# Kernel tuning notes

Hardware: AMD Instinct MI355X
Metric: run time of the kernel (lower is better)

The kernel has to match this reference:

```python
import jax, jax.numpy as jnp
import numpy as np


def setup_inputs() -> dict:
    key = jax.random.key(0)
    k1, k2 = jax.random.split(key)
    outputs = jax.random.normal(k1, (256, 8192, 3), dtype=jnp.float32)
    targets = jax.random.normal(k2, (256, 8192, 3), dtype=jnp.float32)
    return {"outputs": outputs, "targets": targets}


def reference(outputs, targets):
    # Flatten to rows of 3-vectors, per the original reshape((-1, 3)).
    o = outputs.reshape(-1, 3)
    t = targets.reshape(-1, 3)
    # Row-wise dot and norms, angle via acos, then mean.
    dot = jnp.sum(o * t, axis=-1)
    cos = dot / (jnp.linalg.norm(o, axis=-1) * jnp.linalg.norm(t, axis=-1))
    angles = jnp.arccos(cos)
    return jnp.mean(angles)
```

## Files before the change

kernel.cpp:

```cpp
#include <hip/hip_runtime.h>
#include <math.h>

#define N_ROWS   (256 * 8192)
#define BLOCK    256
#define ROWS_PER_THREAD 4
#define GRID     (N_ROWS / (BLOCK * ROWS_PER_THREAD))
#define F4_PER_BLOCK (BLOCK * 3)

__device__ __forceinline__ int swz(int j) { return j ^ ((j >> 3) & 7); }

__device__ __forceinline__ float acos_fast(float x) {
    float ax = fabsf(x);
    float s  = sqrtf(fmaxf(0.0f, 1.0f - ax));
    float p  = fmaf(ax, -0.0187293f, 0.0742610f);
    p = fmaf(ax, p, -0.2121144f);
    p = fmaf(ax, p, 1.5707288f);
    float r = s * p;
    return (x >= 0.0f) ? r : (3.14159265358979f - r);
}

__global__ __launch_bounds__(BLOCK) void angle_partial(
    const float* __restrict__ o,
    const float* __restrict__ t,
    float* __restrict__ partial)
{
    __shared__ float4 so[F4_PER_BLOCK];
    __shared__ float4 st[F4_PER_BLOCK];

    const int tx  = threadIdx.x;
    const int bid = blockIdx.x;
    const long base4 = (long)bid * F4_PER_BLOCK;
    const float4* o4 = reinterpret_cast<const float4*>(o);
    const float4* t4 = reinterpret_cast<const float4*>(t);

#pragma unroll
    for (int k = 0; k < 3; ++k) {
        int j = k * BLOCK + tx;
        so[swz(j)] = o4[base4 + j];
        st[swz(j)] = t4[base4 + j];
    }
    __syncthreads();

    float4 a0 = so[swz(3 * tx + 0)];
    float4 a1 = so[swz(3 * tx + 1)];
    float4 a2 = so[swz(3 * tx + 2)];
    float4 b0 = st[swz(3 * tx + 0)];
    float4 b1 = st[swz(3 * tx + 1)];
    float4 b2 = st[swz(3 * tx + 2)];

    float ox[4] = {a0.x, a0.w, a1.z, a2.y};
    float oy[4] = {a0.y, a1.x, a1.w, a2.z};
    float oz[4] = {a0.z, a1.y, a2.x, a2.w};
    float tx_[4] = {b0.x, b0.w, b1.z, b2.y};
    float ty_[4] = {b0.y, b1.x, b1.w, b2.z};
    float tz_[4] = {b0.z, b1.y, b2.x, b2.w};

    float s = 0.0f;
#pragma unroll
    for (int r = 0; r < 4; ++r) {
        float dot = ox[r] * tx_[r] + oy[r] * ty_[r] + oz[r] * tz_[r];
        float no2 = ox[r] * ox[r] + oy[r] * oy[r] + oz[r] * oz[r];
        float nt2 = tx_[r] * tx_[r] + ty_[r] * ty_[r] + tz_[r] * tz_[r];
        float c = dot * rsqrtf(no2) * rsqrtf(nt2);
        c = fminf(1.0f, fmaxf(-1.0f, c));
        s += acos_fast(c);
    }

#pragma unroll
    for (int off = 32; off > 0; off >>= 1)
        s += __shfl_down(s, off, 64);

    __shared__ float waves[BLOCK / 64];
    const int lane = tx & 63;
    const int wid  = tx >> 6;
    if (lane == 0) waves[wid] = s;
    __syncthreads();

    if (tx == 0) {
        float bs = 0.0f;
#pragma unroll
        for (int w = 0; w < BLOCK / 64; ++w) bs += waves[w];
        partial[bid] = bs;
    }
}

__global__ __launch_bounds__(BLOCK) void angle_final(
    const float* __restrict__ partial,
    float* __restrict__ out)
{
    float s = 0.0f;
    for (int i = threadIdx.x; i < GRID; i += BLOCK)
        s += partial[i];

#pragma unroll
    for (int off = 32; off > 0; off >>= 1)
        s += __shfl_down(s, off, 64);

    __shared__ float waves[BLOCK / 64];
    const int lane = threadIdx.x & 63;
    const int wid  = threadIdx.x >> 6;
    if (lane == 0) waves[wid] = s;
    __syncthreads();

    if (threadIdx.x == 0) {
        float total = 0.0f;
#pragma unroll
        for (int w = 0; w < BLOCK / 64; ++w) total += waves[w];
        out[0] = total / (float)N_ROWS;
    }
}

extern "C" void kernel_launch(void* const* d_in, const int* in_sizes, int n_in,
                              void* d_out, int out_size, void* d_ws, size_t ws_size,
                              hipStream_t stream)
{
    const float* outputs = (const float*)d_in[0];
    const float* targets = (const float*)d_in[1];
    float* out = (float*)d_out;
    float* partial = (float*)d_ws;

    angle_partial<<<GRID, BLOCK, 0, stream>>>(outputs, targets, partial);
    angle_final<<<1, BLOCK, 0, stream>>>(partial, out);
}
```

Baseline: 16.62 us.

## Drop LDS staging, load rows directly, and fuse final reduction via atomics

Each thread now loads six contiguous float4s per input straight from global memory (8 rows) instead of staging through swizzled shared memory, so the block-level syncthreads and LDS traffic go away. The second reduction kernel is replaced by a float atomic add of each block's scaled sum into the output, preceded by a memset. This costs per-thread strided (non-coalesced across lanes) loads and a nondeterministic summation order, and keeps two launches (memset plus kernel).

```diff
diff --git a/kernel.cpp b/kernel.cpp
--- a/kernel.cpp
+++ b/kernel.cpp
@@ -3,11 +3,9 @@
 
 #define N_ROWS   (256 * 8192)
 #define BLOCK    256
-#define ROWS_PER_THREAD 4
+#define ROWS_PER_THREAD 8
 #define GRID     (N_ROWS / (BLOCK * ROWS_PER_THREAD))
-#define F4_PER_BLOCK (BLOCK * 3)
-
-__device__ __forceinline__ int swz(int j) { return j ^ ((j >> 3) & 7); }
+#define F4_PER_THREAD 6
 
 __device__ __forceinline__ float acos_fast(float x) {
     float ax = fabsf(x);
@@ -19,52 +17,53 @@
     return (x >= 0.0f) ? r : (3.14159265358979f - r);
 }
 
-__global__ __launch_bounds__(BLOCK) void angle_partial(
-    const float* __restrict__ o,
-    const float* __restrict__ t,
-    float* __restrict__ partial)
-{
-    __shared__ float4 so[F4_PER_BLOCK];
-    __shared__ float4 st[F4_PER_BLOCK];
-
-    const int tx  = threadIdx.x;
-    const int bid = blockIdx.x;
-    const long base4 = (long)bid * F4_PER_BLOCK;
-    const float4* o4 = reinterpret_cast<const float4*>(o);
-    const float4* t4 = reinterpret_cast<const float4*>(t);
-
-#pragma unroll
-    for (int k = 0; k < 3; ++k) {
-        int j = k * BLOCK + tx;
-        so[swz(j)] = o4[base4 + j];
-        st[swz(j)] = t4[base4 + j];
-    }
-    __syncthreads();
-
-    float4 a0 = so[swz(3 * tx + 0)];
-    float4 a1 = so[swz(3 * tx + 1)];
-    float4 a2 = so[swz(3 * tx + 2)];
-    float4 b0 = st[swz(3 * tx + 0)];
-    float4 b1 = st[swz(3 * tx + 1)];
-    float4 b2 = st[swz(3 * tx + 2)];
-
+__device__ __forceinline__ float rows4(float4 a0, float4 a1, float4 a2,
+                                       float4 b0, float4 b1, float4 b2) {
     float ox[4] = {a0.x, a0.w, a1.z, a2.y};
     float oy[4] = {a0.y, a1.x, a1.w, a2.z};
     float oz[4] = {a0.z, a1.y, a2.x, a2.w};
-    float tx_[4] = {b0.x, b0.w, b1.z, b2.y};
-    float ty_[4] = {b0.y, b1.x, b1.w, b2.z};
-    float tz_[4] = {b0.z, b1.y, b2.x, b2.w};
-
+    float txv[4] = {b0.x, b0.w, b1.z, b2.y};
+    float tyv[4] = {b0.y, b1.x, b1.w, b2.z};
+    float tzv[4] = {b0.z, b1.y, b2.x, b2.w};
     float s = 0.0f;
 #pragma unroll
     for (int r = 0; r < 4; ++r) {
-        float dot = ox[r] * tx_[r] + oy[r] * ty_[r] + oz[r] * tz_[r];
+        float dot = ox[r] * txv[r] + oy[r] * tyv[r] + oz[r] * tzv[r];
         float no2 = ox[r] * ox[r] + oy[r] * oy[r] + oz[r] * oz[r];
-        float nt2 = tx_[r] * tx_[r] + ty_[r] * ty_[r] + tz_[r] * tz_[r];
+        float nt2 = txv[r] * txv[r] + tyv[r] * tyv[r] + tzv[r] * tzv[r];
         float c = dot * rsqrtf(no2) * rsqrtf(nt2);
         c = fminf(1.0f, fmaxf(-1.0f, c));
         s += acos_fast(c);
     }
+    return s;
+}
+
+__global__ __launch_bounds__(BLOCK) void angle_main(
+    const float* __restrict__ o,
+    const float* __restrict__ t,
+    float* __restrict__ out)
+{
+    const int tx  = threadIdx.x;
+    const int gid = blockIdx.x * BLOCK + tx;
+    const long base4 = (long)gid * F4_PER_THREAD;
+    const float4* o4 = reinterpret_cast<const float4*>(o);
+    const float4* t4 = reinterpret_cast<const float4*>(t);
+
+    float4 a0 = o4[base4 + 0];
+    float4 a1 = o4[base4 + 1];
+    float4 a2 = o4[base4 + 2];
+    float4 a3 = o4[base4 + 3];
+    float4 a4 = o4[base4 + 4];
+    float4 a5 = o4[base4 + 5];
+    float4 b0 = t4[base4 + 0];
+    float4 b1 = t4[base4 + 1];
+    float4 b2 = t4[base4 + 2];
+    float4 b3 = t4[base4 + 3];
+    float4 b4 = t4[base4 + 4];
+    float4 b5 = t4[base4 + 5];
+
+    float s = rows4(a0, a1, a2, b0, b1, b2)
+            + rows4(a3, a4, a5, b3, b4, b5);
 
 #pragma unroll
     for (int off = 32; off > 0; off >>= 1)
@@ -80,33 +79,8 @@
         float bs = 0.0f;
 #pragma unroll
         for (int w = 0; w < BLOCK / 64; ++w) bs += waves[w];
-        partial[bid] = bs;
-    }
-}
-
-__global__ __launch_bounds__(BLOCK) void angle_final(
-    const float* __restrict__ partial,
-    float* __restrict__ out)
-{
-    float s = 0.0f;
-    for (int i = threadIdx.x; i < GRID; i += BLOCK)
-        s += partial[i];
-
-#pragma unroll
-    for (int off = 32; off > 0; off >>= 1)
-        s += __shfl_down(s, off, 64);
-
-    __shared__ float waves[BLOCK / 64];
-    const int lane = threadIdx.x & 63;
-    const int wid  = threadIdx.x >> 6;
-    if (lane == 0) waves[wid] = s;
-    __syncthreads();
-
-    if (threadIdx.x == 0) {
-        float total = 0.0f;
-#pragma unroll
-        for (int w = 0; w < BLOCK / 64; ++w) total += waves[w];
-        out[0] = total / (float)N_ROWS;
+        __hip_atomic_fetch_add(out, bs * (1.0f / (float)N_ROWS),
+                               __ATOMIC_RELAXED, __HIP_MEMORY_SCOPE_AGENT);
     }
 }
 
@@ -117,8 +91,7 @@
     const float* outputs = (const float*)d_in[0];
     const float* targets = (const float*)d_in[1];
     float* out = (float*)d_out;
-    float* partial = (float*)d_ws;
 
-    angle_partial<<<GRID, BLOCK, 0, stream>>>(outputs, targets, partial);
-    angle_final<<<1, BLOCK, 0, stream>>>(partial, out);
+    hipMemsetAsync(out, 0, sizeof(float), stream);
+    angle_main<<<GRID, BLOCK, 0, stream>>>(outputs, targets, out);
 }
```

New measurement: 28.69 us. 1.73x slower.
